# Performance work log

Hardware: AMD Instinct MI355X
Metric: run time of the kernel (lower is better)

## Reference

```python
import jax, jax.numpy as jnp
import numpy as np

B, T, D = 4, 4096, 1024
E, C, O = 8, 1024, 512  # experts, capacity per expert, per-expert out features


def setup_inputs() -> dict:
    key = jax.random.key(0)
    k1, k2, k3, k4 = jax.random.split(key, 4)
    x = jax.random.normal(k1, (B, T, D), dtype=jnp.float32)
    expert_indices = jax.random.randint(k2, (B, E, C), 0, T)
    # nn.Linear(in, out) weight is (out, in) = (E*O, D); reshape -> (E, O, D)
    bound = 1.0 / np.sqrt(D)
    weight = jax.random.uniform(k3, (E, O, D), dtype=jnp.float32, minval=-bound, maxval=bound)
    bias = jax.random.uniform(k4, (E, O), dtype=jnp.float32, minval=-bound, maxval=bound)
    return {"x": x, "expert_indices": expert_indices, "weight": weight, "bias": bias}


def reference(x, expert_indices, weight, bias):
    # gather_experts: select C tokens per (batch, expert) -> (B, E, C, D)
    b_idx = jnp.arange(x.shape[0])[:, None, None]
    selected = x[b_idx, expert_indices]  # (B, E, C, D)
    # per-expert grouped GEMM + bias
    out = jnp.einsum('becd,eod->beco', selected, weight)
    out = out + bias[None, :, None, :]
    return out
```

## Files before the change

kernel.cpp:

```cpp
#include <hip/hip_runtime.h>
#include <stdint.h>

#define Bdim 4
#define Tdim 4096
#define Ddim 1024
#define Edim 8
#define Cdim 1024
#define Odim 512

using bf16x8 = __attribute__((ext_vector_type(8))) __bf16;
using f32x4  = __attribute__((ext_vector_type(4))) float;

__device__ __forceinline__ unsigned short f2bf(float f) {
  unsigned int u = __float_as_uint(f);
  u += 0x7fffu + ((u >> 16) & 1u);
  return (unsigned short)(u >> 16);
}

__global__ void cast_f32_to_bf16(const float* __restrict__ xin,
                                 const float* __restrict__ win,
                                 unsigned short* __restrict__ outp,
                                 int nx4, int ntot4) {
  int i = blockIdx.x * blockDim.x + threadIdx.x;
  if (i >= ntot4) return;
  float4 v;
  if (i < nx4) v = reinterpret_cast<const float4*>(xin)[i];
  else         v = reinterpret_cast<const float4*>(win)[i - nx4];
  ushort4 o;
  o.x = f2bf(v.x); o.y = f2bf(v.y); o.z = f2bf(v.z); o.w = f2bf(v.w);
  reinterpret_cast<ushort4*>(outp)[i] = o;
}

__device__ __forceinline__ void async_copy16(const unsigned short* g,
                                             unsigned short* l) {
  __builtin_amdgcn_global_load_lds(
      (__attribute__((address_space(1))) unsigned int*)g,
      (__attribute__((address_space(3))) unsigned int*)l, 16, 0, 0);
}

__global__ __launch_bounds__(256) void moe_mfma_gemm(
    const unsigned short* __restrict__ xbf,
    const unsigned short* __restrict__ wbf,
    const int* __restrict__ idx,
    const float* __restrict__ bias,
    float* __restrict__ out) {
  __shared__ __align__(16) unsigned short sA[128 * 64];
  __shared__ __align__(16) unsigned short sB[128 * 64];
  __shared__ int sTok[128];

  const int bid = blockIdx.x;
  const int e = bid & 7;
  const int r = bid >> 3;
  const int nt = r & 3;
  const int mt = (r >> 2) & 7;
  const int b = r >> 5;
  const int be = b * 8 + e;

  const int tid = threadIdx.x;
  const int lane = tid & 63;
  const int wid = tid >> 6;
  const int wm = wid >> 1;
  const int wn = wid & 1;

  if (tid < 128) sTok[tid] = idx[be * Cdim + mt * 128 + tid];
  __syncthreads();

  const int rsub = lane >> 3;
  const int kcol = (((lane & 7) ^ rsub) * 8);
  const unsigned short* gA[4];
  const unsigned short* gB[4];
#pragma unroll
  for (int i = 0; i < 4; ++i) {
    const int rr = wid * 32 + i * 8 + rsub;
    gA[i] = xbf + ((size_t)(b * Tdim + sTok[rr])) * Ddim + kcol;
    gB[i] = wbf + ((size_t)(e * Odim + nt * 128 + rr)) * Ddim + kcol;
  }

  f32x4 acc[4][4];
#pragma unroll
  for (int im = 0; im < 4; ++im)
#pragma unroll
    for (int in = 0; in < 4; ++in) acc[im][in] = (f32x4){0.f, 0.f, 0.f, 0.f};

  const int fr = lane & 15;
  const int fkc = lane >> 4;
  const int sw = fr & 7;

  for (int k0 = 0; k0 < Ddim; k0 += 64) {
#pragma unroll
    for (int i = 0; i < 4; ++i) {
      async_copy16(gA[i] + k0, &sA[(wid * 32 + i * 8) * 64]);
      async_copy16(gB[i] + k0, &sB[(wid * 32 + i * 8) * 64]);
    }
    __syncthreads();
#pragma unroll
    for (int kb = 0; kb < 2; ++kb) {
      const int ko = ((kb * 4 + fkc) ^ sw) * 8;
      bf16x8 af[4], bfr[4];
#pragma unroll
      for (int im = 0; im < 4; ++im)
        af[im] = *(const bf16x8*)&sA[(size_t)(wm * 64 + im * 16 + fr) * 64 + ko];
#pragma unroll
      for (int in = 0; in < 4; ++in)
        bfr[in] = *(const bf16x8*)&sB[(size_t)(wn * 64 + in * 16 + fr) * 64 + ko];
#pragma unroll
      for (int im = 0; im < 4; ++im)
#pragma unroll
        for (int in = 0; in < 4; ++in)
          acc[im][in] = __builtin_amdgcn_mfma_f32_16x16x32_bf16(
              af[im], bfr[in], acc[im][in], 0, 0, 0);
    }
    __syncthreads();
  }

  float bv[4];
#pragma unroll
  for (int in = 0; in < 4; ++in)
    bv[in] = bias[e * Odim + nt * 128 + wn * 64 + in * 16 + fr];

  const int crow0 = (lane >> 4) * 4;
  float* outBase = out + (size_t)be * (Cdim * Odim) + (size_t)(mt * 128) * Odim + nt * 128;
#pragma unroll
  for (int im = 0; im < 4; ++im) {
    float* pr = outBase + (size_t)(wm * 64 + im * 16 + crow0) * Odim;
#pragma unroll
    for (int in = 0; in < 4; ++in) {
      float* p = pr + wn * 64 + in * 16 + fr;
#pragma unroll
      for (int r4 = 0; r4 < 4; ++r4) p[(size_t)r4 * Odim] = acc[im][in][r4] + bv[in];
    }
  }
}

extern "C" void kernel_launch(void* const* d_in, const int* in_sizes, int n_in,
                              void* d_out, int out_size, void* d_ws, size_t ws_size,
                              hipStream_t stream) {
  const float* x = (const float*)d_in[0];
  const int* idx = (const int*)d_in[1];
  const float* w = (const float*)d_in[2];
  const float* bias = (const float*)d_in[3];
  float* out = (float*)d_out;

  unsigned short* xbf = (unsigned short*)d_ws;
  unsigned short* wbf = xbf + (size_t)Bdim * Tdim * Ddim;

  const int nx4 = Bdim * Tdim * Ddim / 4;
  const int ntot4 = nx4 + Edim * Odim * Ddim / 4;
  cast_f32_to_bf16<<<(ntot4 + 255) / 256, 256, 0, stream>>>(x, w, xbf, nx4, ntot4);

  moe_mfma_gemm<<<1024, 256, 0, stream>>>(xbf, wbf, idx, bias, out);
}
```

Measured before the change: 169.0 us.

## Use 256x256 tiles with 8 waves and double-buffered quadrant-pipelined loads

```diff
diff --git a/kernel.cpp b/kernel.cpp
--- a/kernel.cpp
+++ b/kernel.cpp
@@ -7,6 +7,7 @@
 #define Edim 8
 #define Cdim 1024
 #define Odim 512
+#define KT 16
 
 using bf16x8 = __attribute__((ext_vector_type(8))) __bf16;
 using f32x4  = __attribute__((ext_vector_type(4))) float;
@@ -38,98 +39,202 @@
       (__attribute__((address_space(3))) unsigned int*)l, 16, 0, 0);
 }
 
-__global__ __launch_bounds__(256) void moe_mfma_gemm(
+#define FENCE() asm volatile("" ::: "memory")
+#define BAR()   do { FENCE(); __builtin_amdgcn_s_barrier(); FENCE(); } while (0)
+
+__global__ __launch_bounds__(512) void moe_mfma_gemm(
     const unsigned short* __restrict__ xbf,
     const unsigned short* __restrict__ wbf,
     const int* __restrict__ idx,
     const float* __restrict__ bias,
     float* __restrict__ out) {
-  __shared__ __align__(16) unsigned short sA[128 * 64];
-  __shared__ __align__(16) unsigned short sB[128 * 64];
-  __shared__ int sTok[128];
+  __shared__ __align__(16) unsigned short sA[2][256][64];
+  __shared__ __align__(16) unsigned short sB[2][256][64];
 
   const int bid = blockIdx.x;
-  const int e = bid & 7;
-  const int r = bid >> 3;
-  const int nt = r & 3;
-  const int mt = (r >> 2) & 7;
-  const int b = r >> 5;
-  const int be = b * 8 + e;
-
-  const int tid = threadIdx.x;
+  const int e   = bid & 7;
+  const int rr_ = bid >> 3;
+  const int nt  = rr_ & 1;
+  const int mt  = (rr_ >> 1) & 3;
+  const int bb  = rr_ >> 3;
+  const int be  = bb * Edim + e;
+
+  const int tid  = threadIdx.x;
   const int lane = tid & 63;
-  const int wid = tid >> 6;
-  const int wm = wid >> 1;
-  const int wn = wid & 1;
-
-  if (tid < 128) sTok[tid] = idx[be * Cdim + mt * 128 + tid];
-  __syncthreads();
+  const int wid  = tid >> 6;
+  const int rw   = wid >> 2;
+  const int cw   = wid & 3;
 
   const int rsub = lane >> 3;
-  const int kcol = (((lane & 7) ^ rsub) * 8);
-  const unsigned short* gA[4];
-  const unsigned short* gB[4];
-#pragma unroll
-  for (int i = 0; i < 4; ++i) {
-    const int rr = wid * 32 + i * 8 + rsub;
-    gA[i] = xbf + ((size_t)(b * Tdim + sTok[rr])) * Ddim + kcol;
-    gB[i] = wbf + ((size_t)(e * Odim + nt * 128 + rr)) * Ddim + kcol;
+  const int kcol = ((lane & 7) ^ rsub) * 8;
+
+  const unsigned short* pA[2][2];
+#pragma unroll
+  for (int h = 0; h < 2; ++h)
+#pragma unroll
+    for (int i = 0; i < 2; ++i) {
+      const int rr  = h * 128 + wid * 16 + i * 8 + rsub;
+      const int tok = idx[be * Cdim + mt * 256 + rr];
+      pA[h][i] = xbf + ((size_t)(bb * Tdim + tok)) * Ddim + kcol;
+    }
+  const unsigned short* pB00 =
+      wbf + ((size_t)(e * Odim + nt * 256 + wid * 16 + rsub)) * Ddim + kcol;
+  asm volatile("s_waitcnt vmcnt(0)" ::: "memory");
+
+#define STAGE_A(slot, h, koff) do {                                          \
+    async_copy16(pA[h][0] + (koff), &sA[slot][(h)*128 + wid*16    ][0]);     \
+    async_copy16(pA[h][1] + (koff), &sA[slot][(h)*128 + wid*16 + 8][0]);     \
+  } while (0)
+#define STAGE_B(slot, h, koff) do {                                          \
+    async_copy16(pB00 + (h)*131072 + (koff),                                 \
+                 &sB[slot][(h)*128 + wid*16    ][0]);                        \
+    async_copy16(pB00 + (h)*131072 + 8192 + (koff),                          \
+                 &sB[slot][(h)*128 + wid*16 + 8][0]);                        \
+  } while (0)
+
+  STAGE_A(0, 0, 0);
+  STAGE_B(0, 0, 0);
+  STAGE_B(0, 1, 0);
+  STAGE_A(0, 1, 0);
+  STAGE_A(1, 0, 64);
+  STAGE_B(1, 0, 64);
+  STAGE_B(1, 1, 64);
+  asm volatile("s_waitcnt vmcnt(6)" ::: "memory");
+  __builtin_amdgcn_s_barrier();
+  FENCE();
+
+  const int fr  = lane & 15;
+  const int fkc = lane >> 4;
+  const int sw  = fr & 7;
+
+  f32x4 acc[2][2][4][2];
+#pragma unroll
+  for (int a = 0; a < 2; ++a)
+#pragma unroll
+    for (int bq = 0; bq < 2; ++bq)
+#pragma unroll
+      for (int im = 0; im < 4; ++im)
+#pragma unroll
+        for (int in = 0; in < 2; ++in)
+          acc[a][bq][im][in] = (f32x4){0.f, 0.f, 0.f, 0.f};
+
+  bf16x8 af[4][2], bf0[2][2], bf1[2][2];
+
+  for (int kt = 0; kt < KT; ++kt) {
+    const int slot  = kt & 1;
+    const int nslot = slot ^ 1;
+    const int k1 = (kt + 1) * 64;
+    const int k2 = (kt + 2) * 64;
+    const bool g1 = (kt + 1 < KT);
+    const bool g2 = (kt + 2 < KT);
+
+#pragma unroll
+    for (int im = 0; im < 4; ++im)
+#pragma unroll
+      for (int kk = 0; kk < 2; ++kk)
+        af[im][kk] = *(const bf16x8*)
+            &sA[slot][rw*64 + im*16 + fr][((kk*4 + fkc) ^ sw) * 8];
+#pragma unroll
+    for (int in = 0; in < 2; ++in)
+#pragma unroll
+      for (int kk = 0; kk < 2; ++kk)
+        bf0[in][kk] = *(const bf16x8*)
+            &sB[slot][cw*32 + in*16 + fr][((kk*4 + fkc) ^ sw) * 8];
+    if (g1) STAGE_A(nslot, 1, k1);
+    BAR();
+    __builtin_amdgcn_s_setprio(1);
+#pragma unroll
+    for (int im = 0; im < 4; ++im)
+#pragma unroll
+      for (int in = 0; in < 2; ++in)
+#pragma unroll
+        for (int kk = 0; kk < 2; ++kk)
+          acc[0][0][im][in] = __builtin_amdgcn_mfma_f32_16x16x32_bf16(
+              af[im][kk], bf0[in][kk], acc[0][0][im][in], 0, 0, 0);
+    __builtin_amdgcn_s_setprio(0);
+    BAR();
+
+#pragma unroll
+    for (int in = 0; in < 2; ++in)
+#pragma unroll
+      for (int kk = 0; kk < 2; ++kk)
+        bf1[in][kk] = *(const bf16x8*)
+            &sB[slot][128 + cw*32 + in*16 + fr][((kk*4 + fkc) ^ sw) * 8];
+    if (g2) STAGE_A(slot, 0, k2);
+    BAR();
+    __builtin_amdgcn_s_setprio(1);
+#pragma unroll
+    for (int im = 0; im < 4; ++im)
+#pragma unroll
+      for (int in = 0; in < 2; ++in)
+#pragma unroll
+        for (int kk = 0; kk < 2; ++kk)
+          acc[0][1][im][in] = __builtin_amdgcn_mfma_f32_16x16x32_bf16(
+              af[im][kk], bf1[in][kk], acc[0][1][im][in], 0, 0, 0);
+    __builtin_amdgcn_s_setprio(0);
+    BAR();
+
+#pragma unroll
+    for (int im = 0; im < 4; ++im)
+#pragma unroll
+      for (int kk = 0; kk < 2; ++kk)
+        af[im][kk] = *(const bf16x8*)
+            &sA[slot][128 + rw*64 + im*16 + fr][((kk*4 + fkc) ^ sw) * 8];
+    if (g2) STAGE_B(slot, 0, k2);
+    BAR();
+    __builtin_amdgcn_s_setprio(1);
+#pragma unroll
+    for (int im = 0; im < 4; ++im)
+#pragma unroll
+      for (int in = 0; in < 2; ++in)
+#pragma unroll
+        for (int kk = 0; kk < 2; ++kk)
+          acc[1][1][im][in] = __builtin_amdgcn_mfma_f32_16x16x32_bf16(
+              af[im][kk], bf1[in][kk], acc[1][1][im][in], 0, 0, 0);
+    __builtin_amdgcn_s_setprio(0);
+    BAR();
+
+#pragma unroll
+    for (int z = 0; z < 1; ++z) { }
+    if (g2) STAGE_B(slot, 1, k2);
+    BAR();
+    __builtin_amdgcn_s_setprio(1);
+#pragma unroll
+    for (int im = 0; im < 4; ++im)
+#pragma unroll
+      for (int in = 0; in < 2; ++in)
+#pragma unroll
+        for (int kk = 0; kk < 2; ++kk)
+          acc[1][0][im][in] = __builtin_amdgcn_mfma_f32_16x16x32_bf16(
+              af[im][kk], bf0[in][kk], acc[1][0][im][in], 0, 0, 0);
+    __builtin_amdgcn_s_setprio(0);
+    if (kt == KT - 2)      asm volatile("s_waitcnt vmcnt(0)" ::: "memory");
+    else if (kt <  KT - 2) asm volatile("s_waitcnt vmcnt(6)" ::: "memory");
+    BAR();
   }
-
-  f32x4 acc[4][4];
-#pragma unroll
-  for (int im = 0; im < 4; ++im)
-#pragma unroll
-    for (int in = 0; in < 4; ++in) acc[im][in] = (f32x4){0.f, 0.f, 0.f, 0.f};
-
-  const int fr = lane & 15;
-  const int fkc = lane >> 4;
-  const int sw = fr & 7;
-
-  for (int k0 = 0; k0 < Ddim; k0 += 64) {
-#pragma unroll
-    for (int i = 0; i < 4; ++i) {
-      async_copy16(gA[i] + k0, &sA[(wid * 32 + i * 8) * 64]);
-      async_copy16(gB[i] + k0, &sB[(wid * 32 + i * 8) * 64]);
+#undef STAGE_A
+#undef STAGE_B
+
+  const int crow0 = (lane >> 4) * 4;
+  float* outBase = out + (size_t)be * (Cdim * Odim)
+                 + (size_t)(mt * 256) * Odim + nt * 256;
+#pragma unroll
+  for (int a = 0; a < 2; ++a)
+#pragma unroll
+    for (int im = 0; im < 4; ++im) {
+      float* prow = outBase + (size_t)(a*128 + rw*64 + im*16 + crow0) * Odim;
+#pragma unroll
+      for (int bq = 0; bq < 2; ++bq)
+#pragma unroll
+        for (int in = 0; in < 2; ++in) {
+          const int col  = bq*128 + cw*32 + in*16 + fr;
+          const float bv = bias[e * Odim + nt * 256 + col];
+          float* p = prow + col;
+#pragma unroll
+          for (int r4 = 0; r4 < 4; ++r4)
+            p[(size_t)r4 * Odim] = acc[a][bq][im][in][r4] + bv;
+        }
     }
-    __syncthreads();
-#pragma unroll
-    for (int kb = 0; kb < 2; ++kb) {
-      const int ko = ((kb * 4 + fkc) ^ sw) * 8;
-      bf16x8 af[4], bfr[4];
-#pragma unroll
-      for (int im = 0; im < 4; ++im)
-        af[im] = *(const bf16x8*)&sA[(size_t)(wm * 64 + im * 16 + fr) * 64 + ko];
-#pragma unroll
-      for (int in = 0; in < 4; ++in)
-        bfr[in] = *(const bf16x8*)&sB[(size_t)(wn * 64 + in * 16 + fr) * 64 + ko];
-#pragma unroll
-      for (int im = 0; im < 4; ++im)
-#pragma unroll
-        for (int in = 0; in < 4; ++in)
-          acc[im][in] = __builtin_amdgcn_mfma_f32_16x16x32_bf16(
-              af[im], bfr[in], acc[im][in], 0, 0, 0);
-    }
-    __syncthreads();
-  }
-
-  float bv[4];
-#pragma unroll
-  for (int in = 0; in < 4; ++in)
-    bv[in] = bias[e * Odim + nt * 128 + wn * 64 + in * 16 + fr];
-
-  const int crow0 = (lane >> 4) * 4;
-  float* outBase = out + (size_t)be * (Cdim * Odim) + (size_t)(mt * 128) * Odim + nt * 128;
-#pragma unroll
-  for (int im = 0; im < 4; ++im) {
-    float* pr = outBase + (size_t)(wm * 64 + im * 16 + crow0) * Odim;
-#pragma unroll
-    for (int in = 0; in < 4; ++in) {
-      float* p = pr + wn * 64 + in * 16 + fr;
-#pragma unroll
-      for (int r4 = 0; r4 < 4; ++r4) p[(size_t)r4 * Odim] = acc[im][in][r4] + bv[in];
-    }
-  }
 }
 
 extern "C" void kernel_launch(void* const* d_in, const int* in_sizes, int n_in,
@@ -148,5 +253,5 @@
   const int ntot4 = nx4 + Edim * Odim * Ddim / 4;
   cast_f32_to_bf16<<<(ntot4 + 255) / 256, 256, 0, stream>>>(x, w, xbf, nx4, ntot4);
 
-  moe_mfma_gemm<<<1024, 256, 0, stream>>>(xbf, wbf, idx, bias, out);
-}
+  moe_mfma_gemm<<<256, 512, 0, stream>>>(xbf, wbf, idx, bias, out);
+}
```

New measurement: 169.0 us. Within noise of the previous version (+0.0%).
